# Optimization experiments

Measured on AMD Instinct MI355X. Metric: run time of the kernel, lower is better.

Reference implementation:

```python
import jax, jax.numpy as jnp
import numpy as np

IN_F = 256
OUT_F = 256
H = 4
DH = OUT_F // H  # 64
N = 6144


def setup_inputs() -> dict:
    key = jax.random.key(0)
    ks = jax.random.split(key, 6)
    x = jax.random.normal(ks[0], (N, IN_F), dtype=jnp.float32)
    adj = jax.random.randint(ks[1], (N, N), 0, 2, dtype=jnp.int32)
    # per-head Linear(in_features, d_head): weights [H, IN_F, DH], bias [H, DH]
    W = jax.random.normal(ks[2], (H, IN_F, DH), dtype=jnp.float32) / np.sqrt(IN_F)
    Wb = jax.random.normal(ks[3], (H, DH), dtype=jnp.float32) * 0.01
    # per-head Linear(2*d_head, 1): weights [H, 2*DH], bias [H]
    A = jax.random.normal(ks[4], (H, 2 * DH), dtype=jnp.float32) / np.sqrt(2 * DH)
    Ab = jax.random.normal(ks[5], (H,), dtype=jnp.float32) * 0.01
    return {"x": x, "adj": adj, "W": W, "Wb": Wb, "A": A, "Ab": Ab}


def reference(x, adj, W, Wb, A, Ab):
    # h[h,n,d] = per-head linear projection of node features
    h = jnp.einsum("ni,hid->hnd", x, W) + Wb[:, None, :]
    a_src, a_dst = A[:, :DH], A[:, DH:]
    # score(i,j) = a_src . h_i + a_dst . h_j + b  (decomposed concat-linear)
    s_src = jnp.einsum("hnd,hd->hn", h, a_src) + Ab[:, None]  # [H, N]
    s_dst = jnp.einsum("hnd,hd->hn", h, a_dst)                # [H, N]
    scores = s_src[:, :, None] + s_dst[:, None, :]            # [H, N, N]
    # Faithful to source: non-edges get score 0.0 (not -inf) before softmax
    scores = jnp.where(adj[None, :, :] > 0, scores, 0.0)
    probs = jax.nn.softmax(scores, axis=-1)                   # row softmax
    out = jnp.einsum("hij,hjd->hid", probs, h)                # [H, N, DH]
    # concat heads along feature dim -> [N, H*DH]
    return jnp.transpose(out, (1, 0, 2)).reshape(N, H * DH)
```

## Files before the change

### kernel.cpp

```cpp
#include <hip/hip_runtime.h>
#include <stdint.h>

#define NN 6144
#define NC 576

typedef float f32x4 __attribute__((ext_vector_type(4)));
typedef __bf16 bf16x8v __attribute__((ext_vector_type(8)));

__device__ __forceinline__ unsigned short f2bf(float f) {
  unsigned u = __float_as_uint(f);
  u += 0x7FFFu + ((u >> 16) & 1u);
  return (unsigned short)(u >> 16);
}

__device__ __forceinline__ float bf2f(unsigned short s) {
  unsigned u = (unsigned)s << 16;
  return __uint_as_float(u);
}

__device__ __forceinline__ unsigned char f2e4m3(float f) {
  unsigned u = __float_as_uint(f);
  unsigned sgn = (u >> 24) & 0x80u;
  unsigned au = u & 0x7FFFFFFFu;
  if (au >= 0x43E00000u) return (unsigned char)(sgn | 0x7E);
  if (au < 0x3C800000u) {
    int q = (int)rintf(__uint_as_float(au) * 512.0f);
    return (unsigned char)(sgn | (q >= 8 ? 0x08 : q));
  }
  unsigned r = au + 0x7FFFFu + ((au >> 20) & 1u);
  int e = (int)(r >> 23) - 127;
  unsigned m = (r >> 20) & 7u;
  return (unsigned char)(sgn | ((unsigned)(e + 7) << 3) | m);
}

__device__ __forceinline__ unsigned short pack2(float a, float b) {
  return (unsigned short)f2e4m3(a) | ((unsigned short)f2e4m3(b) << 8);
}

__device__ __forceinline__ void async_load16(const void* g, void* l) {
  __builtin_amdgcn_global_load_lds(
      (__attribute__((address_space(1))) void*)(uintptr_t)g,
      (__attribute__((address_space(3))) void*)(uint32_t)(uintptr_t)l,
      16, 0, 0);
}

__global__ __launch_bounds__(256) void p0s(
    const float* __restrict__ x, const float* __restrict__ W,
    const float* __restrict__ Aw, const float* __restrict__ Wb,
    unsigned short* __restrict__ xsw, unsigned short* __restrict__ wsw,
    float* __restrict__ Acat, float* __restrict__ T)
{
  const int bid = blockIdx.x, t = threadIdx.x;
  if (bid < 8) {
#pragma unroll
    for (int i = 0; i < 4; ++i) {
      const int e = bid * 256 + t + i * 2048;
      const int l = e & 63, kc = (e >> 6) & 7, ct = e >> 9;
      const int c = ct * 16 + (l & 15);
      const int h = c >> 6, d0 = c & 63;
      const int ks = kc * 32 + (l >> 4) * 8;
      const float* src = W + h * 16384 + ks * 64 + d0;
      unsigned uu[4];
#pragma unroll
      for (int j = 0; j < 4; ++j)
        uu[j] = (unsigned)f2bf(src[(2*j) * 64]) | ((unsigned)f2bf(src[(2*j+1) * 64]) << 16);
      *(uint4*)(wsw + (size_t)e * 8) = (uint4){uu[0], uu[1], uu[2], uu[3]};
    }
    return;
  }
  if (bid == 8) {
    T[t] = 0.f;
    const int h = t >> 6, d = t & 63;
    Acat[t]       = Aw[h * 128 + d];
    Acat[256 + t] = Aw[h * 128 + 64 + d];
    Acat[512 + t] = Wb[t];
    return;
  }
  const int tid = (bid - 9) * 256 + t;
#pragma unroll
  for (int i = 0; i < 4; ++i) {
    const int e = tid + i * 49152;
    const int l = e & 63, kc = (e >> 6) & 7, mt = e >> 9;
    const int node = mt * 16 + (l & 15);
    const int ks = kc * 32 + (l >> 4) * 8;
    const float4* xp = (const float4*)(x + (size_t)node * 256 + ks);
    float4 v0 = xp[0], v1 = xp[1];
    uint4 o;
    o.x = (unsigned)f2bf(v0.x) | ((unsigned)f2bf(v0.y) << 16);
    o.y = (unsigned)f2bf(v0.z) | ((unsigned)f2bf(v0.w) << 16);
    o.z = (unsigned)f2bf(v1.x) | ((unsigned)f2bf(v1.y) << 16);
    o.w = (unsigned)f2bf(v1.z) | ((unsigned)f2bf(v1.w) << 16);
    *(uint4*)(xsw + (size_t)e * 8) = o;
  }
}

__global__ __launch_bounds__(256) void k1m(
    const unsigned short* __restrict__ xsw, const unsigned short* __restrict__ wsw,
    const float* __restrict__ Acat, const float* __restrict__ Ab,
    const int* __restrict__ adj, unsigned* __restrict__ bm,
    unsigned char* __restrict__ V8, float* __restrict__ e_src, float* __restrict__ T)
{
  __shared__ unsigned char lv[4][4096];
  __shared__ float lt[256];
  const int t = threadIdx.x;

  if (blockIdx.x >= 192) {
    const int pb = blockIdx.x - 192;
    const int tid = pb * 256 + t;
    const int4* src = (const int4*)adj + (size_t)tid * 8;
    int4 q[8];
#pragma unroll
    for (int j = 0; j < 8; ++j) q[j] = src[j];
    unsigned b = 0;
#pragma unroll
    for (int j = 0; j < 8; ++j) {
      unsigned nib = (unsigned)q[j].x | ((unsigned)q[j].y << 1) |
                     ((unsigned)q[j].z << 2) | ((unsigned)q[j].w << 3);
      b |= nib << (4 * j);
    }
    bm[tid] = b;
    return;
  }

  const int w = t >> 6, l = t & 63;
  const int v = blockIdx.x * 4 + w;
  const int mt = v >> 1, nh = v & 1;
  const int i0 = mt * 16, c0 = nh * 128;
  const int lm = l & 15, lk = l >> 4;

  lt[t] = 0.f;
  __syncthreads();

  f32x4 acc[8];
#pragma unroll
  for (int nt = 0; nt < 8; ++nt) acc[nt] = (f32x4){0.f, 0.f, 0.f, 0.f};

  const unsigned short* ap = xsw + ((size_t)mt * 512 + l) * 8;
  const unsigned short* bp = wsw + ((size_t)nh * 4096 + l) * 8;

#pragma unroll
  for (int kc = 0; kc < 8; ++kc) {
    bf16x8v a = *(const bf16x8v*)(ap + (size_t)kc * 512);
#pragma unroll
    for (int nt = 0; nt < 8; ++nt) {
      bf16x8v b = *(const bf16x8v*)(bp + ((size_t)nt * 512 + kc * 64) * 8);
      acc[nt] = __builtin_amdgcn_mfma_f32_16x16x32_bf16(a, b, acc[nt], 0, 0, 0);
    }
  }

  float asv[8], adv[8];
#pragma unroll
  for (int nt = 0; nt < 8; ++nt) {
    const int cc = c0 + nt * 16 + lm;
    const float wb = Acat[512 + cc];
#pragma unroll
    for (int rr = 0; rr < 4; ++rr) acc[nt][rr] += wb;
    asv[nt] = Acat[cc];
    adv[nt] = Acat[256 + cc];
  }

#pragma unroll
  for (int nt = 0; nt < 8; ++nt)
    atomicAdd(&lt[c0 + nt * 16 + lm], acc[nt][0] + acc[nt][1] + acc[nt][2] + acc[nt][3]);

  float ss[2][4], sd[2][4];
#pragma unroll
  for (int hl = 0; hl < 2; ++hl)
#pragma unroll
    for (int rr = 0; rr < 4; ++rr) {
      float s1 = 0.f, s2 = 0.f;
#pragma unroll
      for (int j = 0; j < 4; ++j) {
        s1 += acc[hl * 4 + j][rr] * asv[hl * 4 + j];
        s2 += acc[hl * 4 + j][rr] * adv[hl * 4 + j];
      }
      ss[hl][rr] = s1; sd[hl][rr] = s2;
    }
#pragma unroll
  for (int off = 1; off < 16; off <<= 1)
#pragma unroll
    for (int hl = 0; hl < 2; ++hl)
#pragma unroll
      for (int rr = 0; rr < 4; ++rr) {
        ss[hl][rr] += __shfl_xor(ss[hl][rr], off);
        sd[hl][rr] += __shfl_xor(sd[hl][rr], off);
      }

  float ed[2][4];
#pragma unroll
  for (int hl = 0; hl < 2; ++hl)
#pragma unroll
    for (int rr = 0; rr < 4; ++rr) ed[hl][rr] = expf(sd[hl][rr]);

  if (lm == 0) {
#pragma unroll
    for (int hl = 0; hl < 2; ++hl) {
      const int hh = nh * 2 + hl;
      const float ab = Ab[hh];
#pragma unroll
      for (int rr = 0; rr < 4; ++rr)
        e_src[(size_t)hh * NN + i0 + lk * 4 + rr] = expf(ss[hl][rr] + ab);
    }
  }

  unsigned char* mylv = lv[w];
#pragma unroll
  for (int nt = 0; nt < 8; ++nt) {
    const int hl = nt >> 2;
    const int d = (nt & 3) * 16 + lm;
    const int lcE = hl * 128 + d;
    const int lcP = lcE + 64;
    *(unsigned short*)(mylv + lcE * 16 + lk * 4)     = pack2(ed[hl][0] * acc[nt][0], ed[hl][1] * acc[nt][1]);
    *(unsigned short*)(mylv + lcE * 16 + lk * 4 + 2) = pack2(ed[hl][2] * acc[nt][2], ed[hl][3] * acc[nt][3]);
    *(unsigned short*)(mylv + lcP * 16 + lk * 4)     = pack2(acc[nt][0], acc[nt][1]);
    *(unsigned short*)(mylv + lcP * 16 + lk * 4 + 2) = pack2(acc[nt][2], acc[nt][3]);
  }
#pragma unroll
  for (int j = 0; j < 4; ++j) {
    const int lc = j * 64 + l;
    uint4 val = *(const uint4*)(mylv + lc * 16);
    *(uint4*)(V8 + (size_t)(nh * 256 + lc) * NN + i0) = val;
  }
  if (lm == 0) {
#pragma unroll
    for (int hl = 0; hl < 2; ++hl) {
      const int hh = nh * 2 + hl;
      unsigned char* pq = V8 + (size_t)(512 + hh) * NN + i0 + lk * 4;
      *(unsigned short*)pq       = pack2(ed[hl][0], ed[hl][1]);
      *(unsigned short*)(pq + 2) = pack2(ed[hl][2], ed[hl][3]);
    }
    if (nh == 0)
      *(unsigned*)(V8 + (size_t)516 * NN + i0 + lk * 4) = 0x38383838u;
  }

  __syncthreads();
  atomicAdd(&T[t], lt[t]);
}

__global__ __launch_bounds__(256, 3) void k2_gemm(
    const unsigned* __restrict__ bm, const unsigned char* __restrict__ V8,
    unsigned short* __restrict__ out2b, float* __restrict__ out2e, int nks)
{
  __shared__ unsigned char lB[2][144 * 128];
  const int t   = threadIdx.x;
  const int cb  = blockIdx.x & 3;
  const int rb  = (blockIdx.x >> 2) & 31;
  const int ks  = blockIdx.x >> 7;
  const int krange = NN / nks;
  const int i0 = rb * 192, n0 = cb * 144, k0 = ks * krange;
  const int w = t >> 6, l = t & 63;
  const int lm = l & 15, lk = l >> 4;

  f32x4 acc[3][9];
#pragma unroll
  for (int mt = 0; mt < 3; ++mt)
#pragma unroll
    for (int nt = 0; nt < 9; ++nt) acc[mt][nt] = (f32x4){0.f, 0.f, 0.f, 0.f};

  int scol[5], sgr[5];
#pragma unroll
  for (int u = 0; u < 5; ++u) {
    const int gi = u * 256 + t;
    scol[u] = gi >> 3;
    sgr[u]  = (gi & 7) ^ (scol[u] & 7);
  }
  const int dbase4 = (1024 + (t & ~63)) * 16;

  const unsigned* gA0 = bm + (size_t)(i0 + w * 48 + lm) * (NN / 32) + (k0 >> 5) + lk;
  const unsigned char* gBb = V8 + (size_t)n0 * NN + k0;

  const int iters = krange / 128;

#define K2_STAGE(BUF, IT)                                                        \
  do {                                                                           \
    const unsigned char* gB = gBb + (IT) * 128;                                  \
    _Pragma("unroll")                                                            \
    for (int u = 0; u < 4; ++u)                                                  \
      async_load16(gB + (size_t)scol[u] * NN + sgr[u] * 16,                      \
                   (char*)lB[BUF] + (size_t)(u * 256 + (t & ~63)) * 16);         \
    if (t < 128)                                                                 \
      async_load16(gB + (size_t)scol[4] * NN + sgr[4] * 16,                      \
                   (char*)lB[BUF] + dbase4);                                     \
  } while (0)

  unsigned bits_c[3], bits_n[3];
  K2_STAGE(0, 0);
#pragma unroll
  for (int mt = 0; mt < 3; ++mt) bits_c[mt] = gA0[(size_t)mt * 16 * (NN / 32)];
  __syncthreads();

  int cur = 0;
  for (int it = 0; it < iters; ++it) {
    if (it + 1 < iters) {
      K2_STAGE(cur ^ 1, it + 1);
#pragma unroll
      for (int mt = 0; mt < 3; ++mt)
        bits_n[mt] = gA0[(size_t)mt * 16 * (NN / 32) + (it + 1) * 4];
    }

    longlong2 afr[3][2];
#pragma unroll
    for (int mt = 0; mt < 3; ++mt) {
      unsigned u[8];
#pragma unroll
      for (int i = 0; i < 8; ++i) {
        unsigned nib = (bits_c[mt] >> (4 * i)) & 0xFu;
        u[i] = ((nib * 0x00204081u) & 0x01010101u) << 3;
      }
      afr[mt][0].x = (long long)(((unsigned long long)u[1] << 32) | u[0]);
      afr[mt][0].y = (long long)(((unsigned long long)u[3] << 32) | u[2]);
      afr[mt][1].x = (long long)(((unsigned long long)u[5] << 32) | u[4]);
      afr[mt][1].y = (long long)(((unsigned long long)u[7] << 32) | u[6]);
    }

#pragma unroll
    for (int b = 0; b < 2; ++b) {
#pragma unroll
      for (int nt = 0; nt < 9; ++nt) {
        const int cc = nt * 16 + lm;
        const int pos = (lk * 2 + b) ^ (cc & 7);
        longlong2 bv = *(const longlong2*)(lB[cur] + cc * 128 + pos * 16);
#pragma unroll
        for (int mt = 0; mt < 3; ++mt) {
          acc[mt][nt] = __builtin_amdgcn_mfma_f32_16x16x32_fp8_fp8(
              afr[mt][b].x, bv.x, acc[mt][nt], 0, 0, 0);
          acc[mt][nt] = __builtin_amdgcn_mfma_f32_16x16x32_fp8_fp8(
              afr[mt][b].y, bv.y, acc[mt][nt], 0, 0, 0);
        }
      }
    }

    if (it + 1 < iters) {
#pragma unroll
      for (int mt = 0; mt < 3; ++mt) bits_c[mt] = bits_n[mt];
    }
    __syncthreads();
    cur ^= 1;
  }
#undef K2_STAGE

  unsigned short* lw = (unsigned short*)((char*)lB[0] + w * 4608);
  float* oe = out2e + (size_t)ks * ((size_t)NN * 64);
  unsigned short* pb = out2b + ((size_t)(ks * 4 + cb) * NN + i0 + w * 48) * 144;
#pragma unroll
  for (int mt = 0; mt < 3; ++mt) {
#pragma unroll
    for (int nt = 0; nt < 9; ++nt) {
      const int coll = nt * 16 + lm;
#pragma unroll
      for (int rr = 0; rr < 4; ++rr)
        lw[(lk * 4 + rr) * 144 + coll] = f2bf(acc[mt][nt][rr] * 64.0f);
      if (cb == 3 && nt >= 5) {
        const int row = i0 + w * 48 + mt * 16 + lk * 4;
#pragma unroll
        for (int rr = 0; rr < 4; ++rr)
          oe[(size_t)(row + rr) * 64 + (n0 + coll - 512)] = acc[mt][nt][rr] * 64.0f;
      }
    }
    const uint4* ls = (const uint4*)((char*)lB[0] + w * 4608);
    char* dst = (char*)(pb + (size_t)mt * 16 * 144);
    for (int s = l; s < 288; s += 64)
      *(uint4*)(dst + s * 16) = ls[s];
  }
}

__global__ __launch_bounds__(256) void k3_final(
    const unsigned short* __restrict__ out2b, const float* __restrict__ out2e,
    const float* __restrict__ e_src, const float* __restrict__ T,
    float* __restrict__ out, int nks)
{
  const int n = blockIdx.x, c = threadIdx.x;
  const int h = c >> 6, d = c & 63;
  const int cS = h * 128 + d, cP = cS + 64;
  const int cbS = cS / 144, ofS = cS % 144;
  const int cbP = cP / 144, ofP = cP % 144;
  float Se = 0.f, Sp = 0.f, E = 0.f, dg = 0.f;
  for (int s = 0; s < nks; ++s) {
    const unsigned short* base = out2b + (size_t)s * 4 * NN * 144;
    Se += bf2f(base[((size_t)cbS * NN + n) * 144 + ofS]);
    Sp += bf2f(base[((size_t)cbP * NN + n) * 144 + ofP]);
    const float* re = out2e + (size_t)s * NN * 64 + (size_t)n * 64;
    E  += re[h];
    dg += re[4];
  }
  float e = e_src[h * NN + n];
  float D = e * E + ((float)NN - dg);
  out[(size_t)n * 256 + c] = (e * Se + (T[c] - Sp)) / D;
}

extern "C" void kernel_launch(void* const* d_in, const int* in_sizes, int n_in,
                              void* d_out, int out_size, void* d_ws, size_t ws_size,
                              hipStream_t stream) {
  const float* x  = (const float*)d_in[0];
  const int*   adj= (const int*)d_in[1];
  const float* W  = (const float*)d_in[2];
  const float* Wb = (const float*)d_in[3];
  const float* Aw = (const float*)d_in[4];
  const float* Ab = (const float*)d_in[5];
  float* out = (float*)d_out;
  char* ws = (char*)d_ws;
  unsigned char* V8 = (unsigned char*)ws;
  float* e_src = (float*)(ws + 3538944);
  float* T     = (float*)(ws + 3637248);
  float* Acat  = (float*)(ws + 3638272);
  unsigned short* wsw = (unsigned short*)(ws + 3641344);
  unsigned short* xsw = (unsigned short*)(ws + 3772416);
  unsigned* bm = (unsigned*)(ws + 6918144);
  unsigned short* out2b = (unsigned short*)(ws + 44666880);
  float* out2e = (float*)(ws + 87134208);

  const size_t slabB = (size_t)4 * NN * 144 * 2;
  const size_t slabE = (size_t)NN * 64 * 4;
  int nks = 2;
  if (ws_size >= 87134208 + 6 * slabE)                    nks = 6;
  else if (ws_size >= 44666880 + 4 * slabB + 4 * slabE)   nks = 4;

  hipLaunchKernelGGL(p0s, dim3(201), dim3(256), 0, stream,
                     x, W, Aw, Wb, xsw, wsw, Acat, T);
  hipLaunchKernelGGL(k1m, dim3(4800), dim3(256), 0, stream,
                     xsw, wsw, Acat, Ab, adj, bm, V8, e_src, T);
  hipLaunchKernelGGL(k2_gemm, dim3(128 * nks), dim3(256), 0, stream, bm, V8, out2b, out2e, nks);
  hipLaunchKernelGGL(k3_final, dim3(NN), dim3(256), 0, stream, out2b, out2e, e_src, T, out, nks);
}
```

Baseline: 275.5 us.

## Fuse x bf16 conversion into projection kernel and retile aggregation GEMM rows

The x-to-bf16 swizzle moves out of the prep kernel and into the projection kernel, which now converts its own 32-node slice straight into shared memory. This removes the xsw global round trip and shrinks the prep launch to 9 blocks. The aggregation GEMM drops from 192 to 128 rows per block (two M tiles per wave), uses 192 blocks per K-split, and caps the K-split at 4 instead of 6. The aim is more blocks, less register pressure and fewer partial slabs, at the cost of less reuse of each B tile and an extra barrier in k1m for the shared LDS buffer.

```diff
diff --git a/kernel.cpp b/kernel.cpp
--- a/kernel.cpp
+++ b/kernel.cpp
@@ -45,10 +45,10 @@
 }
 
 __global__ __launch_bounds__(256) void p0s(
-    const float* __restrict__ x, const float* __restrict__ W,
+    const float* __restrict__ W,
     const float* __restrict__ Aw, const float* __restrict__ Wb,
-    unsigned short* __restrict__ xsw, unsigned short* __restrict__ wsw,
-    float* __restrict__ Acat, float* __restrict__ T)
+    unsigned short* __restrict__ wsw, float* __restrict__ Acat,
+    float* __restrict__ T)
 {
   const int bid = blockIdx.x, t = threadIdx.x;
   if (bid < 8) {
@@ -68,39 +68,20 @@
     }
     return;
   }
-  if (bid == 8) {
-    T[t] = 0.f;
-    const int h = t >> 6, d = t & 63;
-    Acat[t]       = Aw[h * 128 + d];
-    Acat[256 + t] = Aw[h * 128 + 64 + d];
-    Acat[512 + t] = Wb[t];
-    return;
-  }
-  const int tid = (bid - 9) * 256 + t;
-#pragma unroll
-  for (int i = 0; i < 4; ++i) {
-    const int e = tid + i * 49152;
-    const int l = e & 63, kc = (e >> 6) & 7, mt = e >> 9;
-    const int node = mt * 16 + (l & 15);
-    const int ks = kc * 32 + (l >> 4) * 8;
-    const float4* xp = (const float4*)(x + (size_t)node * 256 + ks);
-    float4 v0 = xp[0], v1 = xp[1];
-    uint4 o;
-    o.x = (unsigned)f2bf(v0.x) | ((unsigned)f2bf(v0.y) << 16);
-    o.y = (unsigned)f2bf(v0.z) | ((unsigned)f2bf(v0.w) << 16);
-    o.z = (unsigned)f2bf(v1.x) | ((unsigned)f2bf(v1.y) << 16);
-    o.w = (unsigned)f2bf(v1.z) | ((unsigned)f2bf(v1.w) << 16);
-    *(uint4*)(xsw + (size_t)e * 8) = o;
-  }
+  T[t] = 0.f;
+  const int h = t >> 6, d = t & 63;
+  Acat[t]       = Aw[h * 128 + d];
+  Acat[256 + t] = Aw[h * 128 + 64 + d];
+  Acat[512 + t] = Wb[t];
 }
 
 __global__ __launch_bounds__(256) void k1m(
-    const unsigned short* __restrict__ xsw, const unsigned short* __restrict__ wsw,
+    const float* __restrict__ x, const unsigned short* __restrict__ wsw,
     const float* __restrict__ Acat, const float* __restrict__ Ab,
     const int* __restrict__ adj, unsigned* __restrict__ bm,
     unsigned char* __restrict__ V8, float* __restrict__ e_src, float* __restrict__ T)
 {
-  __shared__ unsigned char lv[4][4096];
+  __shared__ unsigned char lsh[16384];
   __shared__ float lt[256];
   const int t = threadIdx.x;
 
@@ -128,6 +109,26 @@
   const int i0 = mt * 16, c0 = nh * 128;
   const int lm = l & 15, lk = l >> 4;
 
+  {
+    unsigned short* lx = (unsigned short*)lsh;
+    const float* xb = x + (size_t)(blockIdx.x * 32) * 256;
+#pragma unroll
+    for (int j = 0; j < 4; ++j) {
+      const int e = t + j * 256;
+      const int tile = e >> 9, e9 = e & 511;
+      const int el = e9 & 63, kc = e9 >> 6;
+      const int node = tile * 16 + (el & 15);
+      const int ks = kc * 32 + (el >> 4) * 8;
+      const float4* xp = (const float4*)(xb + (size_t)node * 256 + ks);
+      float4 v0 = xp[0], v1 = xp[1];
+      uint4 o;
+      o.x = (unsigned)f2bf(v0.x) | ((unsigned)f2bf(v0.y) << 16);
+      o.y = (unsigned)f2bf(v0.z) | ((unsigned)f2bf(v0.w) << 16);
+      o.z = (unsigned)f2bf(v1.x) | ((unsigned)f2bf(v1.y) << 16);
+      o.w = (unsigned)f2bf(v1.z) | ((unsigned)f2bf(v1.w) << 16);
+      *(uint4*)(lx + (size_t)e * 8) = o;
+    }
+  }
   lt[t] = 0.f;
   __syncthreads();
 
@@ -135,7 +136,7 @@
 #pragma unroll
   for (int nt = 0; nt < 8; ++nt) acc[nt] = (f32x4){0.f, 0.f, 0.f, 0.f};
 
-  const unsigned short* ap = xsw + ((size_t)mt * 512 + l) * 8;
+  const unsigned short* ap = (const unsigned short*)lsh + (((size_t)(w >> 1)) * 512 + l) * 8;
   const unsigned short* bp = wsw + ((size_t)nh * 4096 + l) * 8;
 
 #pragma unroll
@@ -203,7 +204,9 @@
     }
   }
 
-  unsigned char* mylv = lv[w];
+  __syncthreads();
+
+  unsigned char* mylv = lsh + w * 4096;
 #pragma unroll
   for (int nt = 0; nt < 8; ++nt) {
     const int hl = nt >> 2;
@@ -243,17 +246,18 @@
 {
   __shared__ unsigned char lB[2][144 * 128];
   const int t   = threadIdx.x;
-  const int cb  = blockIdx.x & 3;
-  const int rb  = (blockIdx.x >> 2) & 31;
-  const int ks  = blockIdx.x >> 7;
+  const int ks  = blockIdx.x / 192;
+  const int r   = blockIdx.x - ks * 192;
+  const int cb  = r & 3;
+  const int rb  = r >> 2;
   const int krange = NN / nks;
-  const int i0 = rb * 192, n0 = cb * 144, k0 = ks * krange;
+  const int i0 = rb * 128, n0 = cb * 144, k0 = ks * krange;
   const int w = t >> 6, l = t & 63;
   const int lm = l & 15, lk = l >> 4;
 
-  f32x4 acc[3][9];
-#pragma unroll
-  for (int mt = 0; mt < 3; ++mt)
+  f32x4 acc[2][9];
+#pragma unroll
+  for (int mt = 0; mt < 2; ++mt)
 #pragma unroll
     for (int nt = 0; nt < 9; ++nt) acc[mt][nt] = (f32x4){0.f, 0.f, 0.f, 0.f};
 
@@ -266,7 +270,7 @@
   }
   const int dbase4 = (1024 + (t & ~63)) * 16;
 
-  const unsigned* gA0 = bm + (size_t)(i0 + w * 48 + lm) * (NN / 32) + (k0 >> 5) + lk;
+  const unsigned* gA0 = bm + (size_t)(i0 + w * 32 + lm) * (NN / 32) + (k0 >> 5) + lk;
   const unsigned char* gBb = V8 + (size_t)n0 * NN + k0;
 
   const int iters = krange / 128;
@@ -283,10 +287,10 @@
                    (char*)lB[BUF] + dbase4);                                     \
   } while (0)
 
-  unsigned bits_c[3], bits_n[3];
+  unsigned bits_c[2], bits_n[2];
   K2_STAGE(0, 0);
 #pragma unroll
-  for (int mt = 0; mt < 3; ++mt) bits_c[mt] = gA0[(size_t)mt * 16 * (NN / 32)];
+  for (int mt = 0; mt < 2; ++mt) bits_c[mt] = gA0[(size_t)mt * 16 * (NN / 32)];
   __syncthreads();
 
   int cur = 0;
@@ -294,13 +298,13 @@
     if (it + 1 < iters) {
       K2_STAGE(cur ^ 1, it + 1);
 #pragma unroll
-      for (int mt = 0; mt < 3; ++mt)
+      for (int mt = 0; mt < 2; ++mt)
         bits_n[mt] = gA0[(size_t)mt * 16 * (NN / 32) + (it + 1) * 4];
     }
 
-    longlong2 afr[3][2];
-#pragma unroll
-    for (int mt = 0; mt < 3; ++mt) {
+    longlong2 afr[2][2];
+#pragma unroll
+    for (int mt = 0; mt < 2; ++mt) {
       unsigned u[8];
 #pragma unroll
       for (int i = 0; i < 8; ++i) {
@@ -321,7 +325,7 @@
         const int pos = (lk * 2 + b) ^ (cc & 7);
         longlong2 bv = *(const longlong2*)(lB[cur] + cc * 128 + pos * 16);
 #pragma unroll
-        for (int mt = 0; mt < 3; ++mt) {
+        for (int mt = 0; mt < 2; ++mt) {
           acc[mt][nt] = __builtin_amdgcn_mfma_f32_16x16x32_fp8_fp8(
               afr[mt][b].x, bv.x, acc[mt][nt], 0, 0, 0);
           acc[mt][nt] = __builtin_amdgcn_mfma_f32_16x16x32_fp8_fp8(
@@ -332,7 +336,7 @@
 
     if (it + 1 < iters) {
 #pragma unroll
-      for (int mt = 0; mt < 3; ++mt) bits_c[mt] = bits_n[mt];
+      for (int mt = 0; mt < 2; ++mt) bits_c[mt] = bits_n[mt];
     }
     __syncthreads();
     cur ^= 1;
@@ -341,9 +345,9 @@
 
   unsigned short* lw = (unsigned short*)((char*)lB[0] + w * 4608);
   float* oe = out2e + (size_t)ks * ((size_t)NN * 64);
-  unsigned short* pb = out2b + ((size_t)(ks * 4 + cb) * NN + i0 + w * 48) * 144;
-#pragma unroll
-  for (int mt = 0; mt < 3; ++mt) {
+  unsigned short* pb = out2b + ((size_t)(ks * 4 + cb) * NN + i0 + w * 32) * 144;
+#pragma unroll
+  for (int mt = 0; mt < 2; ++mt) {
 #pragma unroll
     for (int nt = 0; nt < 9; ++nt) {
       const int coll = nt * 16 + lm;
@@ -351,7 +355,7 @@
       for (int rr = 0; rr < 4; ++rr)
         lw[(lk * 4 + rr) * 144 + coll] = f2bf(acc[mt][nt][rr] * 64.0f);
       if (cb == 3 && nt >= 5) {
-        const int row = i0 + w * 48 + mt * 16 + lk * 4;
+        const int row = i0 + w * 32 + mt * 16 + lk * 4;
 #pragma unroll
         for (int rr = 0; rr < 4; ++rr)
           oe[(size_t)(row + rr) * 64 + (n0 + coll - 512)] = acc[mt][nt][rr] * 64.0f;
@@ -404,7 +408,6 @@
   float* T     = (float*)(ws + 3637248);
   float* Acat  = (float*)(ws + 3638272);
   unsigned short* wsw = (unsigned short*)(ws + 3641344);
-  unsigned short* xsw = (unsigned short*)(ws + 3772416);
   unsigned* bm = (unsigned*)(ws + 6918144);
   unsigned short* out2b = (unsigned short*)(ws + 44666880);
   float* out2e = (float*)(ws + 87134208);
@@ -412,13 +415,12 @@
   const size_t slabB = (size_t)4 * NN * 144 * 2;
   const size_t slabE = (size_t)NN * 64 * 4;
   int nks = 2;
-  if (ws_size >= 87134208 + 6 * slabE)                    nks = 6;
-  else if (ws_size >= 44666880 + 4 * slabB + 4 * slabE)   nks = 4;
-
-  hipLaunchKernelGGL(p0s, dim3(201), dim3(256), 0, stream,
-                     x, W, Aw, Wb, xsw, wsw, Acat, T);
+  if (ws_size >= 44666880 + 4 * slabB + 4 * slabE)  nks = 4;
+
+  hipLaunchKernelGGL(p0s, dim3(9), dim3(256), 0, stream,
+                     W, Aw, Wb, wsw, Acat, T);
   hipLaunchKernelGGL(k1m, dim3(4800), dim3(256), 0, stream,
-                     xsw, wsw, Acat, Ab, adj, bm, V8, e_src, T);
-  hipLaunchKernelGGL(k2_gemm, dim3(128 * nks), dim3(256), 0, stream, bm, V8, out2b, out2e, nks);
+                     x, wsw, Acat, Ab, adj, bm, V8, e_src, T);
+  hipLaunchKernelGGL(k2_gemm, dim3(192 * nks), dim3(256), 0, stream, bm, V8, out2b, out2e, nks);
   hipLaunchKernelGGL(k3_final, dim3(NN), dim3(256), 0, stream, out2b, out2e, e_src, T, out, nks);
 }
```

Result: no change. 271.7 us (-1.4%).
